# Optimization experiments

Hardware: AMD Instinct MI355X
Metric: run time of the kernel (lower is better)

The kernel has to match this reference:

```python
import jax, jax.numpy as jnp
import numpy as np

N = 100_000      # nodes
E = 1_600_000    # edges
IN, H, OUT = 128, 64, 32


def _gcn_edges(edge_index, n):
    """Add self-loops and compute symmetric GCN normalization (PyG gcn_norm)."""
    src, dst = edge_index[0], edge_index[1]
    loops = jnp.arange(n, dtype=src.dtype)
    src = jnp.concatenate([src, loops])
    dst = jnp.concatenate([dst, loops])
    deg = jax.ops.segment_sum(jnp.ones_like(dst, jnp.float32), dst, num_segments=n)
    dinv = jnp.where(deg > 0, jax.lax.rsqrt(deg), 0.0)
    norm = dinv[src] * dinv[dst]          # [E+N]
    return src, dst, norm


def _gcn_conv(x, src, dst, norm, W, b, n):
    h = x @ W.T                           # dense transform [n, out]
    msg = h[src] * norm[:, None]          # gather + scale per edge
    out = jax.ops.segment_sum(msg, dst, num_segments=n)  # scatter-add
    return out + b


def setup_inputs() -> dict:
    key = jax.random.key(0)
    k1, k2, k3, k4 = jax.random.split(key, 4)
    x = jax.random.normal(k1, (N, IN), dtype=jnp.float32)
    edge_index = jax.random.randint(k2, (2, E), 0, N, dtype=jnp.int32)
    # xavier_normal_: std = sqrt(2 / (fan_in + fan_out))
    W1 = jax.random.normal(k3, (H, IN), dtype=jnp.float32) * np.sqrt(2.0 / (IN + H))
    b1 = jnp.zeros((H,), dtype=jnp.float32)
    W2 = jax.random.normal(k4, (OUT, H), dtype=jnp.float32) * np.sqrt(2.0 / (H + OUT))
    b2 = jnp.zeros((OUT,), dtype=jnp.float32)
    return {"x": x, "edge_index": edge_index, "W1": W1, "b1": b1, "W2": W2, "b2": b2}


def reference(x, edge_index, W1, b1, W2, b2):
    n = x.shape[0]
    src, dst, norm = _gcn_edges(edge_index, n)
    h = _gcn_conv(x, src, dst, norm, W1, b1, n)
    h = jax.nn.relu(h)
    out = _gcn_conv(h, src, dst, norm, W2, b2, n)
    return out
```

## Files before the change

### kernel.cpp

```cpp
#include <hip/hip_runtime.h>

#define THREADS 256
#define G1 256
#define MAXNB 4096
#define BCAP 2688

using bf16x8 = __attribute__((ext_vector_type(8))) short;
using f32x4 = __attribute__((ext_vector_type(4))) float;

static __device__ __forceinline__ unsigned short f2bf(float f) {
  unsigned u = __float_as_uint(f);
  unsigned r = (u + 0x7fff + ((u >> 16) & 1)) >> 16;
  return (unsigned short)r;
}
static __device__ __forceinline__ float bflo(unsigned w) {
  return __uint_as_float(w << 16);
}
static __device__ __forceinline__ float bfhi(unsigned w) {
  return __uint_as_float(w & 0xffff0000u);
}
static __device__ __forceinline__ unsigned pk2(float a, float b) {
  return (unsigned)f2bf(a) | ((unsigned)f2bf(b) << 16);
}


__global__ void k_scan_chunk(const int* __restrict__ cnt, int* __restrict__ rp,
                             int* __restrict__ bsum, int m) {
  __shared__ int s[256];
  int b = blockIdx.x, t = threadIdx.x;
  int base = b * 1024 + t * 4;
  int v[4];
  int sum = 0;
#pragma unroll
  for (int k = 0; k < 4; ++k) {
    int i = base + k;
    v[k] = (i < m) ? cnt[i] : 0;
    sum += v[k];
  }
  s[t] = sum;
  __syncthreads();
  int mine = sum;
  for (int off = 1; off < 256; off <<= 1) {
    int y = (t >= off) ? s[t - off] : 0;
    __syncthreads();
    s[t] += y;
    __syncthreads();
  }
  int run = s[t] - mine;
  if (t == 255) bsum[b] = s[255];
#pragma unroll
  for (int k = 0; k < 4; ++k) {
    int i = base + k;
    if (i <= m) rp[i] = run;
    run += v[k];
  }
}

__global__ void k_scan_bsum(int* __restrict__ bsum, int nb) {
  __shared__ int s[256];
  int t = threadIdx.x;
  int v = (t < nb) ? bsum[t] : 0;
  s[t] = v;
  __syncthreads();
  for (int off = 1; off < 256; off <<= 1) {
    int y = (t >= off) ? s[t - off] : 0;
    __syncthreads();
    s[t] += y;
    __syncthreads();
  }
  if (t < nb) bsum[t] = s[t] - v;
}


__launch_bounds__(256)
__global__ void k_pcount(const int* __restrict__ dst, int* __restrict__ C, int e,
                         int NB, int chunk, unsigned* __restrict__ h1b,
                         unsigned* __restrict__ h2b, int n) {
  __shared__ int h[MAXNB];
  int blk = blockIdx.x, t = threadIdx.x;
  if (blk == 0) {
    if (t < 32) h1b[(size_t)n * 32 + t] = 0u;
    else if (t < 48) h2b[(size_t)n * 16 + (t - 32)] = 0u;
  }
  for (int i = t; i < NB; i += 256) h[i] = 0;
  __syncthreads();
  int beg = blk * chunk;
  int stop = min(e, beg + chunk);
  for (int j = beg + t; j < stop; j += 256) atomicAdd(&h[dst[j] >> 7], 1);
  __syncthreads();
  for (int i = t; i < NB; i += 256) C[i * G1 + blk] = h[i];
}

__launch_bounds__(256)
__global__ void k_partition(const int* __restrict__ src, const int* __restrict__ dst,
                            const int* __restrict__ Cs, const int* __restrict__ bsum,
                            int* __restrict__ bpack, int e, int NB, int chunk) {
  __shared__ int cur[MAXNB];
  int blk = blockIdx.x, t = threadIdx.x;
  for (int i = t; i < NB; i += 256) {
    int f = i * G1 + blk;
    cur[i] = Cs[f] + bsum[f >> 10];
  }
  __syncthreads();
  int beg = blk * chunk;
  int stop = min(e, beg + chunk);
  for (int j = beg + t; j < stop; j += 256) {
    int d = dst[j];
    int b = d >> 7;
    int pos = atomicAdd(&cur[b], 1);
    bpack[pos] = (src[j] << 7) | (d & 127);
  }
}

__launch_bounds__(256)
__global__ void k_bucket_csr(const int* __restrict__ bpack, const int* __restrict__ Cs,
                             const int* __restrict__ bsum, int* __restrict__ rp,
                             float* __restrict__ dinv, int* __restrict__ csr_src,
                             int n, int e, int NB) {
  __shared__ int cl[128];
  __shared__ int cur[128];
  __shared__ int buf[BCAP];
  int blk = blockIdx.x, t = threadIdx.x;
  int fb = blk * G1;
  int base = Cs[fb] + bsum[fb >> 10];
  int end;
  if (blk == NB - 1) {
    end = e;
  } else {
    int fe = (blk + 1) * G1;
    end = Cs[fe] + bsum[fe >> 10];
  }
  int cnt = end - base;
  if (t < 128) cl[t] = 0;
  __syncthreads();
  if (cnt <= BCAP) {
    for (int j = base + t; j < end; j += 256) {
      int p = bpack[j];
      buf[j - base] = p;
      atomicAdd(&cl[p & 127], 1);
    }
  } else {
    for (int j = base + t; j < end; j += 256) atomicAdd(&cl[bpack[j] & 127], 1);
  }
  __syncthreads();
  int own = (t < 128) ? cl[t] : 0;
  for (int off = 1; off < 128; off <<= 1) {
    int y = (t >= off && t < 128) ? cl[t - off] : 0;
    __syncthreads();
    if (t < 128) cl[t] += y;
    __syncthreads();
  }
  if (t < 128) {
    int excl = cl[t] - own;
    int v = (blk << 7) + t;
    if (v < n) {
      rp[v] = base + excl;
      dinv[v] = rsqrtf((float)own + 1.0f);
    }
    cur[t] = base + excl;
  }
  __syncthreads();
  if (cnt <= BCAP) {
    for (int j = t; j < cnt; j += 256) {
      int p = buf[j];
      int pos = atomicAdd(&cur[p & 127], 1);
      csr_src[pos] = p >> 7;
    }
  } else {
    for (int j = base + t; j < end; j += 256) {
      int p = bpack[j];
      int pos = atomicAdd(&cur[p & 127], 1);
      csr_src[pos] = p >> 7;
    }
  }
  if (blk == 0 && t == 0) rp[n] = e;
}


__launch_bounds__(256)
__global__ void k_gemm1(const float* __restrict__ x, const float* __restrict__ W1,
                        const float* __restrict__ dinv, unsigned short* __restrict__ h1b,
                        int n) {
  __shared__ uint4 sXb[64 * 16];
  __shared__ uint4 sWb[64 * 16];
  __shared__ __align__(16) unsigned short sOut[64 * 64];
  int t = threadIdx.x;
  const float4* x4 = (const float4*)x;
  const float4* W14 = (const float4*)W1;
  int rbase = blockIdx.x * 64;
#pragma unroll
  for (int p = 0; p < 4; ++p) {
    int q = t + 256 * p;
    int r = q >> 4, s = q & 15;
    int gr = rbase + r;
    float4 v0 = make_float4(0.f, 0.f, 0.f, 0.f), v1 = v0;
    if (gr < n) {
      v0 = x4[(size_t)gr * 32 + s * 2];
      v1 = x4[(size_t)gr * 32 + s * 2 + 1];
    }
    uint4 pk;
    pk.x = pk2(v0.x, v0.y);
    pk.y = pk2(v0.z, v0.w);
    pk.z = pk2(v1.x, v1.y);
    pk.w = pk2(v1.z, v1.w);
    sXb[r * 16 + (s ^ (r & 15))] = pk;
  }
#pragma unroll
  for (int p = 0; p < 4; ++p) {
    int q = t + 256 * p;
    int c = q >> 4, s = q & 15;
    float4 v0 = W14[c * 32 + s * 2];
    float4 v1 = W14[c * 32 + s * 2 + 1];
    uint4 pk;
    pk.x = pk2(v0.x, v0.y);
    pk.y = pk2(v0.z, v0.w);
    pk.z = pk2(v1.x, v1.y);
    pk.w = pk2(v1.z, v1.w);
    sWb[c * 16 + (s ^ (c & 15))] = pk;
  }
  __syncthreads();
  int lane = t & 63;
  int w = t >> 6;
  int l16 = lane & 15, quad = lane >> 4;
  int arow = w * 16 + l16;
  f32x4 acc0 = {0.f, 0.f, 0.f, 0.f};
  f32x4 acc1 = {0.f, 0.f, 0.f, 0.f};
  f32x4 acc2 = {0.f, 0.f, 0.f, 0.f};
  f32x4 acc3 = {0.f, 0.f, 0.f, 0.f};
#pragma unroll
  for (int kc = 0; kc < 4; ++kc) {
    int slot = kc * 4 + quad;
    uint4 ua = sXb[arow * 16 + (slot ^ (arow & 15))];
    bf16x8 a = *(bf16x8*)&ua;
    uint4 ub0 = sWb[(0 + l16) * 16 + (slot ^ l16)];
    uint4 ub1 = sWb[(16 + l16) * 16 + (slot ^ l16)];
    uint4 ub2 = sWb[(32 + l16) * 16 + (slot ^ l16)];
    uint4 ub3 = sWb[(48 + l16) * 16 + (slot ^ l16)];
    acc0 = __builtin_amdgcn_mfma_f32_16x16x32_bf16(a, *(bf16x8*)&ub0, acc0, 0, 0, 0);
    acc1 = __builtin_amdgcn_mfma_f32_16x16x32_bf16(a, *(bf16x8*)&ub1, acc1, 0, 0, 0);
    acc2 = __builtin_amdgcn_mfma_f32_16x16x32_bf16(a, *(bf16x8*)&ub2, acc2, 0, 0, 0);
    acc3 = __builtin_amdgcn_mfma_f32_16x16x32_bf16(a, *(bf16x8*)&ub3, acc3, 0, 0, 0);
  }
  float dvr[4];
#pragma unroll
  for (int r = 0; r < 4; ++r) {
    int grow = rbase + w * 16 + quad * 4 + r;
    dvr[r] = (grow < n) ? dinv[grow] : 0.f;
  }
#pragma unroll
  for (int r = 0; r < 4; ++r) {
    int rl = w * 16 + quad * 4 + r;
    sOut[rl * 64 + 0 + l16] = f2bf(acc0[r] * dvr[r]);
    sOut[rl * 64 + 16 + l16] = f2bf(acc1[r] * dvr[r]);
    sOut[rl * 64 + 32 + l16] = f2bf(acc2[r] * dvr[r]);
    sOut[rl * 64 + 48 + l16] = f2bf(acc3[r] * dvr[r]);
  }
  __syncthreads();
#pragma unroll
  for (int p = 0; p < 2; ++p) {
    int q = t + 256 * p;
    int r = q >> 3, s = q & 7;
    int gr = rbase + r;
    if (gr < n)
      *(uint4*)&h1b[(size_t)gr * 64 + s * 8] = *(uint4*)&sOut[r * 64 + s * 8];
  }
}


__launch_bounds__(256)
__global__ void k_agg1(const unsigned* __restrict__ h1p, const float* __restrict__ dinv,
                       const int* __restrict__ rp, const int* __restrict__ csr_src,
                       unsigned* __restrict__ agg1b, int n) {
  int gid = blockIdx.x * 256 + threadIdx.x;
  int v = gid >> 4, f4 = gid & 15;
  if (v >= n) return;
  const uint2* h1q = (const uint2*)h1p;
  int beg = rp[v], end = rp[v + 1];
  uint2 w0 = h1q[(size_t)v * 16 + f4];
  float acc[8][4];
#pragma unroll
  for (int k = 0; k < 8; ++k)
#pragma unroll
    for (int c = 0; c < 4; ++c) acc[k][c] = 0.f;
  acc[0][0] = bflo(w0.x);
  acc[0][1] = bfhi(w0.x);
  acc[0][2] = bflo(w0.y);
  acc[0][3] = bfhi(w0.y);
  for (int j = beg; j < end; j += 8) {
    int s[8];
#pragma unroll
    for (int k = 0; k < 8; ++k) s[k] = csr_src[j + k];
#pragma unroll
    for (int k = 1; k < 8; ++k) s[k] = (j + k < end) ? s[k] : n;
    uint2 g[8];
#pragma unroll
    for (int k = 0; k < 8; ++k) g[k] = h1q[(size_t)s[k] * 16 + f4];
#pragma unroll
    for (int k = 0; k < 8; ++k) {
      acc[k][0] += bflo(g[k].x);
      acc[k][1] += bfhi(g[k].x);
      acc[k][2] += bflo(g[k].y);
      acc[k][3] += bfhi(g[k].y);
    }
  }
  float s0 = ((acc[0][0] + acc[1][0]) + (acc[2][0] + acc[3][0])) +
             ((acc[4][0] + acc[5][0]) + (acc[6][0] + acc[7][0]));
  float s1 = ((acc[0][1] + acc[1][1]) + (acc[2][1] + acc[3][1])) +
             ((acc[4][1] + acc[5][1]) + (acc[6][1] + acc[7][1]));
  float s2 = ((acc[0][2] + acc[1][2]) + (acc[2][2] + acc[3][2])) +
             ((acc[4][2] + acc[5][2]) + (acc[6][2] + acc[7][2]));
  float s3 = ((acc[0][3] + acc[1][3]) + (acc[2][3] + acc[3][3])) +
             ((acc[4][3] + acc[5][3]) + (acc[6][3] + acc[7][3]));
  float dv = dinv[v];
  uint2 o;
  o.x = pk2(dv * s0, dv * s1);
  o.y = pk2(dv * s2, dv * s3);
  ((uint2*)agg1b)[(size_t)v * 16 + f4] = o;
}


__launch_bounds__(256)
__global__ void k_gemm2(const unsigned* __restrict__ agg1b, const float* __restrict__ b1,
                        const float* __restrict__ W2, const float* __restrict__ dinv,
                        unsigned short* __restrict__ h2b, int n) {
  __shared__ uint4 sXb[64 * 8];
  __shared__ uint4 sWb[32 * 8];
  __shared__ __align__(16) unsigned short sOut[64 * 32];
  int t = threadIdx.x;
  int rbase = blockIdx.x * 64;
  const uint4* a4 = (const uint4*)agg1b;
  const float4* b14 = (const float4*)b1;
  const float4* W24 = (const float4*)W2;
#pragma unroll
  for (int p = 0; p < 2; ++p) {
    int q = t + 256 * p;
    int r = q >> 3, s = q & 7;
    int gr = rbase + r;
    uint4 o = make_uint4(0u, 0u, 0u, 0u);
    if (gr < n) {
      uint4 a = a4[(size_t)gr * 8 + s];
      float4 blo = b14[s * 2], bhi = b14[s * 2 + 1];
      o.x = pk2(fmaxf(bflo(a.x) + blo.x, 0.f), fmaxf(bfhi(a.x) + blo.y, 0.f));
      o.y = pk2(fmaxf(bflo(a.y) + blo.z, 0.f), fmaxf(bfhi(a.y) + blo.w, 0.f));
      o.z = pk2(fmaxf(bflo(a.z) + bhi.x, 0.f), fmaxf(bfhi(a.z) + bhi.y, 0.f));
      o.w = pk2(fmaxf(bflo(a.w) + bhi.z, 0.f), fmaxf(bfhi(a.w) + bhi.w, 0.f));
    }
    sXb[r * 8 + (s ^ (r & 7))] = o;
  }
  {
    int c = t >> 3, s = t & 7;
    float4 v0 = W24[c * 16 + s * 2];
    float4 v1 = W24[c * 16 + s * 2 + 1];
    uint4 pk;
    pk.x = pk2(v0.x, v0.y);
    pk.y = pk2(v0.z, v0.w);
    pk.z = pk2(v1.x, v1.y);
    pk.w = pk2(v1.z, v1.w);
    sWb[c * 8 + (s ^ (c & 7))] = pk;
  }
  __syncthreads();
  int lane = t & 63;
  int w = t >> 6;
  int l16 = lane & 15, quad = lane >> 4;
  int arow = w * 16 + l16;
  f32x4 acc0 = {0.f, 0.f, 0.f, 0.f};
  f32x4 acc1 = {0.f, 0.f, 0.f, 0.f};
#pragma unroll
  for (int kc = 0; kc < 2; ++kc) {
    int slot = kc * 4 + quad;
    uint4 ua = sXb[arow * 8 + (slot ^ (arow & 7))];
    bf16x8 a = *(bf16x8*)&ua;
    uint4 ub0 = sWb[l16 * 8 + (slot ^ (l16 & 7))];
    uint4 ub1 = sWb[(16 + l16) * 8 + (slot ^ (l16 & 7))];
    acc0 = __builtin_amdgcn_mfma_f32_16x16x32_bf16(a, *(bf16x8*)&ub0, acc0, 0, 0, 0);
    acc1 = __builtin_amdgcn_mfma_f32_16x16x32_bf16(a, *(bf16x8*)&ub1, acc1, 0, 0, 0);
  }
  float dvr[4];
#pragma unroll
  for (int r = 0; r < 4; ++r) {
    int grow = rbase + w * 16 + quad * 4 + r;
    dvr[r] = (grow < n) ? dinv[grow] : 0.f;
  }
#pragma unroll
  for (int r = 0; r < 4; ++r) {
    int rl = w * 16 + quad * 4 + r;
    sOut[rl * 32 + l16] = f2bf(acc0[r] * dvr[r]);
    sOut[rl * 32 + 16 + l16] = f2bf(acc1[r] * dvr[r]);
  }
  __syncthreads();
  {
    int r = t >> 2, s = t & 3;
    int gr = rbase + r;
    if (gr < n)
      *(uint4*)&h2b[(size_t)gr * 32 + s * 8] = *(uint4*)&sOut[r * 32 + s * 8];
  }
}


__launch_bounds__(256)
__global__ void k_agg2(const unsigned* __restrict__ h2p, const float* __restrict__ dinv,
                       const int* __restrict__ rp, const int* __restrict__ csr_src,
                       const float* __restrict__ b2, float* __restrict__ out, int n) {
  int gid = blockIdx.x * 256 + threadIdx.x;
  int v = gid >> 3, f4 = gid & 7;
  if (v >= n) return;
  const uint2* h2q = (const uint2*)h2p;
  int beg = rp[v], end = rp[v + 1];
  uint2 w0 = h2q[(size_t)v * 8 + f4];
  float acc[8][4];
#pragma unroll
  for (int k = 0; k < 8; ++k)
#pragma unroll
    for (int c = 0; c < 4; ++c) acc[k][c] = 0.f;
  acc[0][0] = bflo(w0.x);
  acc[0][1] = bfhi(w0.x);
  acc[0][2] = bflo(w0.y);
  acc[0][3] = bfhi(w0.y);
  for (int j = beg; j < end; j += 8) {
    int s[8];
#pragma unroll
    for (int k = 0; k < 8; ++k) s[k] = csr_src[j + k];
#pragma unroll
    for (int k = 1; k < 8; ++k) s[k] = (j + k < end) ? s[k] : n;
    uint2 g[8];
#pragma unroll
    for (int k = 0; k < 8; ++k) g[k] = h2q[(size_t)s[k] * 8 + f4];
#pragma unroll
    for (int k = 0; k < 8; ++k) {
      acc[k][0] += bflo(g[k].x);
      acc[k][1] += bfhi(g[k].x);
      acc[k][2] += bflo(g[k].y);
      acc[k][3] += bfhi(g[k].y);
    }
  }
  float s0 = ((acc[0][0] + acc[1][0]) + (acc[2][0] + acc[3][0])) +
             ((acc[4][0] + acc[5][0]) + (acc[6][0] + acc[7][0]));
  float s1 = ((acc[0][1] + acc[1][1]) + (acc[2][1] + acc[3][1])) +
             ((acc[4][1] + acc[5][1]) + (acc[6][1] + acc[7][1]));
  float s2 = ((acc[0][2] + acc[1][2]) + (acc[2][2] + acc[3][2])) +
             ((acc[4][2] + acc[5][2]) + (acc[6][2] + acc[7][2]));
  float s3 = ((acc[0][3] + acc[1][3]) + (acc[2][3] + acc[3][3])) +
             ((acc[4][3] + acc[5][3]) + (acc[6][3] + acc[7][3]));
  float dv = dinv[v];
  float4 bv = ((const float4*)b2)[f4];
  float4 o;
  o.x = fmaf(dv, s0, bv.x);
  o.y = fmaf(dv, s1, bv.y);
  o.z = fmaf(dv, s2, bv.z);
  o.w = fmaf(dv, s3, bv.w);
  ((float4*)out)[(size_t)v * 8 + f4] = o;
}


extern "C" void kernel_launch(void* const* d_in, const int* in_sizes, int n_in,
                              void* d_out, int out_size, void* d_ws, size_t ws_size,
                              hipStream_t stream) {
  const float* x = (const float*)d_in[0];
  const int* ei = (const int*)d_in[1];
  const float* W1 = (const float*)d_in[2];
  const float* b1 = (const float*)d_in[3];
  const float* W2 = (const float*)d_in[4];
  const float* b2 = (const float*)d_in[5];
  float* out = (float*)d_out;

  const int n = in_sizes[0] / 128;
  const int e = in_sizes[1] / 2;
  const int* src = ei;
  const int* dst = ei + e;

  const int NB = (n + 127) >> 7;
  const int m = NB * G1;
  const int chunk = (e + G1 - 1) / G1;
  const int NC = (m + 1 + 1023) / 1024;

  char* base = (char*)d_ws;
  size_t off = 0;
  auto alloc = [&](size_t bytes) {
    char* p = base + off;
    off = (off + bytes + 255) & ~(size_t)255;
    return p;
  };
  int* C = (int*)alloc((size_t)m * 4);
  int* Cs = (int*)alloc((size_t)(m + 1) * 4);
  int* bsum = (int*)alloc(1024 * 4);
  int* bpack = (int*)alloc((size_t)e * 4);
  int* rp = (int*)alloc((size_t)(n + 1) * 4);
  int* csr_src = (int*)alloc((size_t)(e + 8) * 4);
  float* dinv = (float*)alloc((size_t)n * 4);
  unsigned short* h1b = (unsigned short*)alloc((size_t)(n + 1) * 64 * 2);
  unsigned* agg1b = (unsigned*)alloc((size_t)n * 64 * 2);
  unsigned short* h2b = (unsigned short*)alloc((size_t)(n + 1) * 32 * 2);

  k_pcount<<<G1, 256, 0, stream>>>(dst, C, e, NB, chunk, (unsigned*)h1b,
                                   (unsigned*)h2b, n);
  k_scan_chunk<<<NC, 256, 0, stream>>>(C, Cs, bsum, m);
  k_scan_bsum<<<1, 256, 0, stream>>>(bsum, NC);
  k_partition<<<G1, 256, 0, stream>>>(src, dst, Cs, bsum, bpack, e, NB, chunk);
  k_bucket_csr<<<NB, 256, 0, stream>>>(bpack, Cs, bsum, rp, dinv, csr_src, n, e, NB);

  k_gemm1<<<(n + 63) / 64, 256, 0, stream>>>(x, W1, dinv, h1b, n);
  {
    long long total = (long long)n * 16;
    k_agg1<<<(int)((total + 255) / 256), 256, 0, stream>>>((const unsigned*)h1b, dinv,
                                                           rp, csr_src, agg1b, n);
  }

  k_gemm2<<<(n + 63) / 64, 256, 0, stream>>>(agg1b, b1, W2, dinv, h2b, n);
  {
    long long total = (long long)n * 8;
    k_agg2<<<(int)((total + 255) / 256), 256, 0, stream>>>((const unsigned*)h2b, dinv,
                                                           rp, csr_src, b2, out, n);
  }
}
```

Baseline: 209.7 us.

## Fuse all GCN stages into one persistent kernel with software grid barriers

```diff
diff --git a/kernel.cpp b/kernel.cpp
--- a/kernel.cpp
+++ b/kernel.cpp
@@ -1,7 +1,6 @@
 #include <hip/hip_runtime.h>
 
-#define THREADS 256
-#define G1 256
+#define GP 256
 #define MAXNB 4096
 #define BCAP 2688
 
@@ -23,432 +22,459 @@
   return (unsigned)f2bf(a) | ((unsigned)f2bf(b) << 16);
 }
 
-
-__global__ void k_scan_chunk(const int* __restrict__ cnt, int* __restrict__ rp,
-                             int* __restrict__ bsum, int m) {
-  __shared__ int s[256];
-  int b = blockIdx.x, t = threadIdx.x;
-  int base = b * 1024 + t * 4;
-  int v[4];
-  int sum = 0;
-#pragma unroll
-  for (int k = 0; k < 4; ++k) {
-    int i = base + k;
-    v[k] = (i < m) ? cnt[i] : 0;
-    sum += v[k];
-  }
-  s[t] = sum;
+static __device__ __forceinline__ void gridbar(int* cnt, int target) {
   __syncthreads();
-  int mine = sum;
-  for (int off = 1; off < 256; off <<= 1) {
-    int y = (t >= off) ? s[t - off] : 0;
+  if (threadIdx.x == 0) {
+    __threadfence();
+    __hip_atomic_fetch_add(cnt, 1, __ATOMIC_RELAXED, __HIP_MEMORY_SCOPE_AGENT);
+    while (__hip_atomic_load(cnt, __ATOMIC_RELAXED, __HIP_MEMORY_SCOPE_AGENT) <
+           target)
+      __builtin_amdgcn_s_sleep(2);
+    __threadfence();
+  }
+  __syncthreads();
+}
+
+
+__global__ void __launch_bounds__(256) k_mega(
+    const float* __restrict__ x, const int* __restrict__ src,
+    const int* __restrict__ dst, const float* __restrict__ W1,
+    const float* __restrict__ b1, const float* __restrict__ W2,
+    const float* __restrict__ b2, int* __restrict__ C, int* __restrict__ Cs,
+    int* __restrict__ bsum, int* __restrict__ bpack, int* __restrict__ rp,
+    int* __restrict__ csr_src, float* __restrict__ dinv,
+    unsigned short* __restrict__ h1b, unsigned short* __restrict__ h2b,
+    float* __restrict__ out, int* __restrict__ barcnt, int n, int e, int NB, int m,
+    int NC, int chunk) {
+  __shared__ __align__(16) char lds_raw[32 * 1024];
+  const int t = threadIdx.x;
+  const int blk = blockIdx.x;
+  const int G = gridDim.x;
+  int bphase = 0;
+
+  if (blk == 0) {
+    unsigned* h1u = (unsigned*)h1b;
+    unsigned* h2u = (unsigned*)h2b;
+    if (t < 32) h1u[(size_t)n * 32 + t] = 0u;
+    else if (t < 48) h2u[(size_t)n * 16 + (t - 32)] = 0u;
+  }
+  {
+    int* h = (int*)lds_raw;
+    for (int pb = blk; pb < GP; pb += G) {
+      __syncthreads();
+      for (int i = t; i < NB; i += 256) h[i] = 0;
+      __syncthreads();
+      int beg = pb * chunk;
+      int stop = min(e, beg + chunk);
+      for (int j = beg + t; j < stop; j += 256) atomicAdd(&h[dst[j] >> 7], 1);
+      __syncthreads();
+      for (int i = t; i < NB; i += 256) C[i * GP + pb] = h[i];
+    }
+  }
+  gridbar(barcnt, ++bphase * G);
+
+  {
+    int* s = (int*)lds_raw;
+    for (int c = blk; c < NC; c += G) {
+      __syncthreads();
+      int base = c * 1024 + t * 4;
+      int v[4];
+      int sum = 0;
+#pragma unroll
+      for (int k = 0; k < 4; ++k) {
+        int i = base + k;
+        v[k] = (i < m) ? C[i] : 0;
+        sum += v[k];
+      }
+      s[t] = sum;
+      __syncthreads();
+      int mine = sum;
+      for (int off = 1; off < 256; off <<= 1) {
+        int y = (t >= off) ? s[t - off] : 0;
+        __syncthreads();
+        s[t] += y;
+        __syncthreads();
+      }
+      int run = s[t] - mine;
+      if (t == 255) bsum[c] = s[255];
+#pragma unroll
+      for (int k = 0; k < 4; ++k) {
+        int i = base + k;
+        if (i <= m) Cs[i] = run;
+        run += v[k];
+      }
+    }
+  }
+  gridbar(barcnt, ++bphase * G);
+
+  int* sb = (int*)lds_raw;
+  {
+    int* ss = sb + 1024;
+    int v4[4];
+    int b4 = t * 4;
+    int sum = 0;
+#pragma unroll
+    for (int k = 0; k < 4; ++k) {
+      int i = b4 + k;
+      v4[k] = (i < NC) ? bsum[i] : 0;
+      sum += v4[k];
+    }
+    ss[t] = sum;
     __syncthreads();
-    s[t] += y;
+    int mine = sum;
+    for (int off = 1; off < 256; off <<= 1) {
+      int y = (t >= off) ? ss[t - off] : 0;
+      __syncthreads();
+      ss[t] += y;
+      __syncthreads();
+    }
+    int run = ss[t] - mine;
+#pragma unroll
+    for (int k = 0; k < 4; ++k) {
+      int i = b4 + k;
+      if (i < NC) sb[i] = run;
+      run += v4[k];
+    }
     __syncthreads();
   }
-  int run = s[t] - mine;
-  if (t == 255) bsum[b] = s[255];
-#pragma unroll
-  for (int k = 0; k < 4; ++k) {
-    int i = base + k;
-    if (i <= m) rp[i] = run;
-    run += v[k];
-  }
-}
-
-__global__ void k_scan_bsum(int* __restrict__ bsum, int nb) {
-  __shared__ int s[256];
-  int t = threadIdx.x;
-  int v = (t < nb) ? bsum[t] : 0;
-  s[t] = v;
-  __syncthreads();
-  for (int off = 1; off < 256; off <<= 1) {
-    int y = (t >= off) ? s[t - off] : 0;
-    __syncthreads();
-    s[t] += y;
-    __syncthreads();
-  }
-  if (t < nb) bsum[t] = s[t] - v;
-}
-
-
-__launch_bounds__(256)
-__global__ void k_pcount(const int* __restrict__ dst, int* __restrict__ C, int e,
-                         int NB, int chunk, unsigned* __restrict__ h1b,
-                         unsigned* __restrict__ h2b, int n) {
-  __shared__ int h[MAXNB];
-  int blk = blockIdx.x, t = threadIdx.x;
-  if (blk == 0) {
-    if (t < 32) h1b[(size_t)n * 32 + t] = 0u;
-    else if (t < 48) h2b[(size_t)n * 16 + (t - 32)] = 0u;
-  }
-  for (int i = t; i < NB; i += 256) h[i] = 0;
-  __syncthreads();
-  int beg = blk * chunk;
-  int stop = min(e, beg + chunk);
-  for (int j = beg + t; j < stop; j += 256) atomicAdd(&h[dst[j] >> 7], 1);
-  __syncthreads();
-  for (int i = t; i < NB; i += 256) C[i * G1 + blk] = h[i];
-}
-
-__launch_bounds__(256)
-__global__ void k_partition(const int* __restrict__ src, const int* __restrict__ dst,
-                            const int* __restrict__ Cs, const int* __restrict__ bsum,
-                            int* __restrict__ bpack, int e, int NB, int chunk) {
-  __shared__ int cur[MAXNB];
-  int blk = blockIdx.x, t = threadIdx.x;
-  for (int i = t; i < NB; i += 256) {
-    int f = i * G1 + blk;
-    cur[i] = Cs[f] + bsum[f >> 10];
-  }
-  __syncthreads();
-  int beg = blk * chunk;
-  int stop = min(e, beg + chunk);
-  for (int j = beg + t; j < stop; j += 256) {
-    int d = dst[j];
-    int b = d >> 7;
-    int pos = atomicAdd(&cur[b], 1);
-    bpack[pos] = (src[j] << 7) | (d & 127);
-  }
-}
-
-__launch_bounds__(256)
-__global__ void k_bucket_csr(const int* __restrict__ bpack, const int* __restrict__ Cs,
-                             const int* __restrict__ bsum, int* __restrict__ rp,
-                             float* __restrict__ dinv, int* __restrict__ csr_src,
-                             int n, int e, int NB) {
-  __shared__ int cl[128];
-  __shared__ int cur[128];
-  __shared__ int buf[BCAP];
-  int blk = blockIdx.x, t = threadIdx.x;
-  int fb = blk * G1;
-  int base = Cs[fb] + bsum[fb >> 10];
-  int end;
-  if (blk == NB - 1) {
-    end = e;
-  } else {
-    int fe = (blk + 1) * G1;
-    end = Cs[fe] + bsum[fe >> 10];
-  }
-  int cnt = end - base;
-  if (t < 128) cl[t] = 0;
-  __syncthreads();
-  if (cnt <= BCAP) {
-    for (int j = base + t; j < end; j += 256) {
-      int p = bpack[j];
-      buf[j - base] = p;
-      atomicAdd(&cl[p & 127], 1);
-    }
-  } else {
-    for (int j = base + t; j < end; j += 256) atomicAdd(&cl[bpack[j] & 127], 1);
-  }
-  __syncthreads();
-  int own = (t < 128) ? cl[t] : 0;
-  for (int off = 1; off < 128; off <<= 1) {
-    int y = (t >= off && t < 128) ? cl[t - off] : 0;
-    __syncthreads();
-    if (t < 128) cl[t] += y;
-    __syncthreads();
-  }
-  if (t < 128) {
-    int excl = cl[t] - own;
-    int v = (blk << 7) + t;
-    if (v < n) {
-      rp[v] = base + excl;
-      dinv[v] = rsqrtf((float)own + 1.0f);
-    }
-    cur[t] = base + excl;
-  }
-  __syncthreads();
-  if (cnt <= BCAP) {
-    for (int j = t; j < cnt; j += 256) {
-      int p = buf[j];
-      int pos = atomicAdd(&cur[p & 127], 1);
-      csr_src[pos] = p >> 7;
-    }
-  } else {
-    for (int j = base + t; j < end; j += 256) {
-      int p = bpack[j];
-      int pos = atomicAdd(&cur[p & 127], 1);
-      csr_src[pos] = p >> 7;
-    }
-  }
-  if (blk == 0 && t == 0) rp[n] = e;
-}
-
-
-__launch_bounds__(256)
-__global__ void k_gemm1(const float* __restrict__ x, const float* __restrict__ W1,
-                        const float* __restrict__ dinv, unsigned short* __restrict__ h1b,
-                        int n) {
-  __shared__ uint4 sXb[64 * 16];
-  __shared__ uint4 sWb[64 * 16];
-  __shared__ __align__(16) unsigned short sOut[64 * 64];
-  int t = threadIdx.x;
-  const float4* x4 = (const float4*)x;
-  const float4* W14 = (const float4*)W1;
-  int rbase = blockIdx.x * 64;
-#pragma unroll
-  for (int p = 0; p < 4; ++p) {
-    int q = t + 256 * p;
-    int r = q >> 4, s = q & 15;
-    int gr = rbase + r;
-    float4 v0 = make_float4(0.f, 0.f, 0.f, 0.f), v1 = v0;
-    if (gr < n) {
-      v0 = x4[(size_t)gr * 32 + s * 2];
-      v1 = x4[(size_t)gr * 32 + s * 2 + 1];
-    }
-    uint4 pk;
-    pk.x = pk2(v0.x, v0.y);
-    pk.y = pk2(v0.z, v0.w);
-    pk.z = pk2(v1.x, v1.y);
-    pk.w = pk2(v1.z, v1.w);
-    sXb[r * 16 + (s ^ (r & 15))] = pk;
-  }
-#pragma unroll
-  for (int p = 0; p < 4; ++p) {
-    int q = t + 256 * p;
-    int c = q >> 4, s = q & 15;
-    float4 v0 = W14[c * 32 + s * 2];
-    float4 v1 = W14[c * 32 + s * 2 + 1];
-    uint4 pk;
-    pk.x = pk2(v0.x, v0.y);
-    pk.y = pk2(v0.z, v0.w);
-    pk.z = pk2(v1.x, v1.y);
-    pk.w = pk2(v1.z, v1.w);
-    sWb[c * 16 + (s ^ (c & 15))] = pk;
-  }
-  __syncthreads();
-  int lane = t & 63;
-  int w = t >> 6;
-  int l16 = lane & 15, quad = lane >> 4;
-  int arow = w * 16 + l16;
-  f32x4 acc0 = {0.f, 0.f, 0.f, 0.f};
-  f32x4 acc1 = {0.f, 0.f, 0.f, 0.f};
-  f32x4 acc2 = {0.f, 0.f, 0.f, 0.f};
-  f32x4 acc3 = {0.f, 0.f, 0.f, 0.f};
-#pragma unroll
-  for (int kc = 0; kc < 4; ++kc) {
-    int slot = kc * 4 + quad;
-    uint4 ua = sXb[arow * 16 + (slot ^ (arow & 15))];
-    bf16x8 a = *(bf16x8*)&ua;
-    uint4 ub0 = sWb[(0 + l16) * 16 + (slot ^ l16)];
-    uint4 ub1 = sWb[(16 + l16) * 16 + (slot ^ l16)];
-    uint4 ub2 = sWb[(32 + l16) * 16 + (slot ^ l16)];
-    uint4 ub3 = sWb[(48 + l16) * 16 + (slot ^ l16)];
-    acc0 = __builtin_amdgcn_mfma_f32_16x16x32_bf16(a, *(bf16x8*)&ub0, acc0, 0, 0, 0);
-    acc1 = __builtin_amdgcn_mfma_f32_16x16x32_bf16(a, *(bf16x8*)&ub1, acc1, 0, 0, 0);
-    acc2 = __builtin_amdgcn_mfma_f32_16x16x32_bf16(a, *(bf16x8*)&ub2, acc2, 0, 0, 0);
-    acc3 = __builtin_amdgcn_mfma_f32_16x16x32_bf16(a, *(bf16x8*)&ub3, acc3, 0, 0, 0);
-  }
-  float dvr[4];
-#pragma unroll
-  for (int r = 0; r < 4; ++r) {
-    int grow = rbase + w * 16 + quad * 4 + r;
-    dvr[r] = (grow < n) ? dinv[grow] : 0.f;
-  }
-#pragma unroll
-  for (int r = 0; r < 4; ++r) {
-    int rl = w * 16 + quad * 4 + r;
-    sOut[rl * 64 + 0 + l16] = f2bf(acc0[r] * dvr[r]);
-    sOut[rl * 64 + 16 + l16] = f2bf(acc1[r] * dvr[r]);
-    sOut[rl * 64 + 32 + l16] = f2bf(acc2[r] * dvr[r]);
-    sOut[rl * 64 + 48 + l16] = f2bf(acc3[r] * dvr[r]);
-  }
-  __syncthreads();
-#pragma unroll
-  for (int p = 0; p < 2; ++p) {
-    int q = t + 256 * p;
-    int r = q >> 3, s = q & 7;
-    int gr = rbase + r;
-    if (gr < n)
-      *(uint4*)&h1b[(size_t)gr * 64 + s * 8] = *(uint4*)&sOut[r * 64 + s * 8];
-  }
-}
-
-
-__launch_bounds__(256)
-__global__ void k_agg1(const unsigned* __restrict__ h1p, const float* __restrict__ dinv,
-                       const int* __restrict__ rp, const int* __restrict__ csr_src,
-                       unsigned* __restrict__ agg1b, int n) {
-  int gid = blockIdx.x * 256 + threadIdx.x;
-  int v = gid >> 4, f4 = gid & 15;
-  if (v >= n) return;
-  const uint2* h1q = (const uint2*)h1p;
-  int beg = rp[v], end = rp[v + 1];
-  uint2 w0 = h1q[(size_t)v * 16 + f4];
-  float acc[8][4];
-#pragma unroll
-  for (int k = 0; k < 8; ++k)
-#pragma unroll
-    for (int c = 0; c < 4; ++c) acc[k][c] = 0.f;
-  acc[0][0] = bflo(w0.x);
-  acc[0][1] = bfhi(w0.x);
-  acc[0][2] = bflo(w0.y);
-  acc[0][3] = bfhi(w0.y);
-  for (int j = beg; j < end; j += 8) {
-    int s[8];
-#pragma unroll
-    for (int k = 0; k < 8; ++k) s[k] = csr_src[j + k];
-#pragma unroll
-    for (int k = 1; k < 8; ++k) s[k] = (j + k < end) ? s[k] : n;
-    uint2 g[8];
-#pragma unroll
-    for (int k = 0; k < 8; ++k) g[k] = h1q[(size_t)s[k] * 16 + f4];
-#pragma unroll
-    for (int k = 0; k < 8; ++k) {
-      acc[k][0] += bflo(g[k].x);
-      acc[k][1] += bfhi(g[k].x);
-      acc[k][2] += bflo(g[k].y);
-      acc[k][3] += bfhi(g[k].y);
-    }
-  }
-  float s0 = ((acc[0][0] + acc[1][0]) + (acc[2][0] + acc[3][0])) +
-             ((acc[4][0] + acc[5][0]) + (acc[6][0] + acc[7][0]));
-  float s1 = ((acc[0][1] + acc[1][1]) + (acc[2][1] + acc[3][1])) +
-             ((acc[4][1] + acc[5][1]) + (acc[6][1] + acc[7][1]));
-  float s2 = ((acc[0][2] + acc[1][2]) + (acc[2][2] + acc[3][2])) +
-             ((acc[4][2] + acc[5][2]) + (acc[6][2] + acc[7][2]));
-  float s3 = ((acc[0][3] + acc[1][3]) + (acc[2][3] + acc[3][3])) +
-             ((acc[4][3] + acc[5][3]) + (acc[6][3] + acc[7][3]));
-  float dv = dinv[v];
-  uint2 o;
-  o.x = pk2(dv * s0, dv * s1);
-  o.y = pk2(dv * s2, dv * s3);
-  ((uint2*)agg1b)[(size_t)v * 16 + f4] = o;
-}
-
-
-__launch_bounds__(256)
-__global__ void k_gemm2(const unsigned* __restrict__ agg1b, const float* __restrict__ b1,
-                        const float* __restrict__ W2, const float* __restrict__ dinv,
-                        unsigned short* __restrict__ h2b, int n) {
-  __shared__ uint4 sXb[64 * 8];
-  __shared__ uint4 sWb[32 * 8];
-  __shared__ __align__(16) unsigned short sOut[64 * 32];
-  int t = threadIdx.x;
-  int rbase = blockIdx.x * 64;
-  const uint4* a4 = (const uint4*)agg1b;
-  const float4* b14 = (const float4*)b1;
-  const float4* W24 = (const float4*)W2;
-#pragma unroll
-  for (int p = 0; p < 2; ++p) {
-    int q = t + 256 * p;
-    int r = q >> 3, s = q & 7;
-    int gr = rbase + r;
-    uint4 o = make_uint4(0u, 0u, 0u, 0u);
-    if (gr < n) {
-      uint4 a = a4[(size_t)gr * 8 + s];
-      float4 blo = b14[s * 2], bhi = b14[s * 2 + 1];
-      o.x = pk2(fmaxf(bflo(a.x) + blo.x, 0.f), fmaxf(bfhi(a.x) + blo.y, 0.f));
-      o.y = pk2(fmaxf(bflo(a.y) + blo.z, 0.f), fmaxf(bfhi(a.y) + blo.w, 0.f));
-      o.z = pk2(fmaxf(bflo(a.z) + bhi.x, 0.f), fmaxf(bfhi(a.z) + bhi.y, 0.f));
-      o.w = pk2(fmaxf(bflo(a.w) + bhi.z, 0.f), fmaxf(bfhi(a.w) + bhi.w, 0.f));
-    }
-    sXb[r * 8 + (s ^ (r & 7))] = o;
-  }
-  {
-    int c = t >> 3, s = t & 7;
-    float4 v0 = W24[c * 16 + s * 2];
-    float4 v1 = W24[c * 16 + s * 2 + 1];
-    uint4 pk;
-    pk.x = pk2(v0.x, v0.y);
-    pk.y = pk2(v0.z, v0.w);
-    pk.z = pk2(v1.x, v1.y);
-    pk.w = pk2(v1.z, v1.w);
-    sWb[c * 8 + (s ^ (c & 7))] = pk;
-  }
-  __syncthreads();
-  int lane = t & 63;
-  int w = t >> 6;
-  int l16 = lane & 15, quad = lane >> 4;
-  int arow = w * 16 + l16;
-  f32x4 acc0 = {0.f, 0.f, 0.f, 0.f};
-  f32x4 acc1 = {0.f, 0.f, 0.f, 0.f};
-#pragma unroll
-  for (int kc = 0; kc < 2; ++kc) {
-    int slot = kc * 4 + quad;
-    uint4 ua = sXb[arow * 8 + (slot ^ (arow & 7))];
-    bf16x8 a = *(bf16x8*)&ua;
-    uint4 ub0 = sWb[l16 * 8 + (slot ^ (l16 & 7))];
-    uint4 ub1 = sWb[(16 + l16) * 8 + (slot ^ (l16 & 7))];
-    acc0 = __builtin_amdgcn_mfma_f32_16x16x32_bf16(a, *(bf16x8*)&ub0, acc0, 0, 0, 0);
-    acc1 = __builtin_amdgcn_mfma_f32_16x16x32_bf16(a, *(bf16x8*)&ub1, acc1, 0, 0, 0);
-  }
-  float dvr[4];
-#pragma unroll
-  for (int r = 0; r < 4; ++r) {
-    int grow = rbase + w * 16 + quad * 4 + r;
-    dvr[r] = (grow < n) ? dinv[grow] : 0.f;
-  }
-#pragma unroll
-  for (int r = 0; r < 4; ++r) {
-    int rl = w * 16 + quad * 4 + r;
-    sOut[rl * 32 + l16] = f2bf(acc0[r] * dvr[r]);
-    sOut[rl * 32 + 16 + l16] = f2bf(acc1[r] * dvr[r]);
-  }
-  __syncthreads();
-  {
-    int r = t >> 2, s = t & 3;
-    int gr = rbase + r;
-    if (gr < n)
-      *(uint4*)&h2b[(size_t)gr * 32 + s * 8] = *(uint4*)&sOut[r * 32 + s * 8];
-  }
-}
-
-
-__launch_bounds__(256)
-__global__ void k_agg2(const unsigned* __restrict__ h2p, const float* __restrict__ dinv,
-                       const int* __restrict__ rp, const int* __restrict__ csr_src,
-                       const float* __restrict__ b2, float* __restrict__ out, int n) {
-  int gid = blockIdx.x * 256 + threadIdx.x;
-  int v = gid >> 3, f4 = gid & 7;
-  if (v >= n) return;
-  const uint2* h2q = (const uint2*)h2p;
-  int beg = rp[v], end = rp[v + 1];
-  uint2 w0 = h2q[(size_t)v * 8 + f4];
-  float acc[8][4];
-#pragma unroll
-  for (int k = 0; k < 8; ++k)
-#pragma unroll
-    for (int c = 0; c < 4; ++c) acc[k][c] = 0.f;
-  acc[0][0] = bflo(w0.x);
-  acc[0][1] = bfhi(w0.x);
-  acc[0][2] = bflo(w0.y);
-  acc[0][3] = bfhi(w0.y);
-  for (int j = beg; j < end; j += 8) {
-    int s[8];
-#pragma unroll
-    for (int k = 0; k < 8; ++k) s[k] = csr_src[j + k];
-#pragma unroll
-    for (int k = 1; k < 8; ++k) s[k] = (j + k < end) ? s[k] : n;
-    uint2 g[8];
-#pragma unroll
-    for (int k = 0; k < 8; ++k) g[k] = h2q[(size_t)s[k] * 8 + f4];
-#pragma unroll
-    for (int k = 0; k < 8; ++k) {
-      acc[k][0] += bflo(g[k].x);
-      acc[k][1] += bfhi(g[k].x);
-      acc[k][2] += bflo(g[k].y);
-      acc[k][3] += bfhi(g[k].y);
-    }
-  }
-  float s0 = ((acc[0][0] + acc[1][0]) + (acc[2][0] + acc[3][0])) +
-             ((acc[4][0] + acc[5][0]) + (acc[6][0] + acc[7][0]));
-  float s1 = ((acc[0][1] + acc[1][1]) + (acc[2][1] + acc[3][1])) +
-             ((acc[4][1] + acc[5][1]) + (acc[6][1] + acc[7][1]));
-  float s2 = ((acc[0][2] + acc[1][2]) + (acc[2][2] + acc[3][2])) +
-             ((acc[4][2] + acc[5][2]) + (acc[6][2] + acc[7][2]));
-  float s3 = ((acc[0][3] + acc[1][3]) + (acc[2][3] + acc[3][3])) +
-             ((acc[4][3] + acc[5][3]) + (acc[6][3] + acc[7][3]));
-  float dv = dinv[v];
-  float4 bv = ((const float4*)b2)[f4];
-  float4 o;
-  o.x = fmaf(dv, s0, bv.x);
-  o.y = fmaf(dv, s1, bv.y);
-  o.z = fmaf(dv, s2, bv.z);
-  o.w = fmaf(dv, s3, bv.w);
-  ((float4*)out)[(size_t)v * 8 + f4] = o;
+
+  {
+    int* cur = (int*)lds_raw + 1280;
+    for (int pb = blk; pb < GP; pb += G) {
+      __syncthreads();
+      for (int i = t; i < NB; i += 256) {
+        int f = i * GP + pb;
+        cur[i] = Cs[f] + sb[f >> 10];
+      }
+      __syncthreads();
+      int beg = pb * chunk;
+      int stop = min(e, beg + chunk);
+      for (int j = beg + t; j < stop; j += 256) {
+        int d = dst[j];
+        int b = d >> 7;
+        int pos = atomicAdd(&cur[b], 1);
+        bpack[pos] = (src[j] << 7) | (d & 127);
+      }
+    }
+  }
+  gridbar(barcnt, ++bphase * G);
+
+  {
+    int* cl = (int*)lds_raw + 1280;
+    int* cur = cl + 128;
+    int* buf = cur + 128;
+    if (blk == 0 && t == 0) rp[n] = e;
+    for (int b = blk; b < NB; b += G) {
+      __syncthreads();
+      int fb = b * GP;
+      int base = Cs[fb] + sb[fb >> 10];
+      int end2 = (b == NB - 1) ? e : (Cs[fb + GP] + sb[(fb + GP) >> 10]);
+      int cnt = end2 - base;
+      if (t < 128) cl[t] = 0;
+      __syncthreads();
+      if (cnt <= BCAP) {
+        for (int j = base + t; j < end2; j += 256) {
+          int p = bpack[j];
+          buf[j - base] = p;
+          atomicAdd(&cl[p & 127], 1);
+        }
+      } else {
+        for (int j = base + t; j < end2; j += 256) atomicAdd(&cl[bpack[j] & 127], 1);
+      }
+      __syncthreads();
+      int own = (t < 128) ? cl[t] : 0;
+      for (int off = 1; off < 128; off <<= 1) {
+        int y = (t >= off && t < 128) ? cl[t - off] : 0;
+        __syncthreads();
+        if (t < 128) cl[t] += y;
+        __syncthreads();
+      }
+      if (t < 128) {
+        int excl = cl[t] - own;
+        int v = (b << 7) + t;
+        if (v < n) {
+          rp[v] = base + excl;
+          dinv[v] = rsqrtf((float)own + 1.0f);
+        }
+        cur[t] = base + excl;
+      }
+      __syncthreads();
+      if (cnt <= BCAP) {
+        for (int j = t; j < cnt; j += 256) {
+          int p = buf[j];
+          int pos = atomicAdd(&cur[p & 127], 1);
+          csr_src[pos] = p >> 7;
+        }
+      } else {
+        for (int j = base + t; j < end2; j += 256) {
+          int p = bpack[j];
+          int pos = atomicAdd(&cur[p & 127], 1);
+          csr_src[pos] = p >> 7;
+        }
+      }
+    }
+  }
+  gridbar(barcnt, ++bphase * G);
+
+  {
+    uint4* sXb = (uint4*)lds_raw;
+    uint4* sWb = sXb + 1024;
+    unsigned short* sOut = (unsigned short*)lds_raw;
+    const float4* x4 = (const float4*)x;
+    const float4* W14 = (const float4*)W1;
+#pragma unroll
+    for (int p = 0; p < 4; ++p) {
+      int q = t + 256 * p;
+      int c = q >> 4, s2 = q & 15;
+      float4 v0 = W14[c * 32 + s2 * 2];
+      float4 v1 = W14[c * 32 + s2 * 2 + 1];
+      uint4 pk;
+      pk.x = pk2(v0.x, v0.y);
+      pk.y = pk2(v0.z, v0.w);
+      pk.z = pk2(v1.x, v1.y);
+      pk.w = pk2(v1.z, v1.w);
+      sWb[c * 16 + (s2 ^ (c & 15))] = pk;
+    }
+    for (int tile = blk; tile * 64 < n; tile += G) {
+      int rbase = tile * 64;
+      __syncthreads();
+#pragma unroll
+      for (int p = 0; p < 4; ++p) {
+        int q = t + 256 * p;
+        int r = q >> 4, s2 = q & 15;
+        int gr = rbase + r;
+        float4 v0 = make_float4(0.f, 0.f, 0.f, 0.f), v1 = v0;
+        if (gr < n) {
+          v0 = x4[(size_t)gr * 32 + s2 * 2];
+          v1 = x4[(size_t)gr * 32 + s2 * 2 + 1];
+        }
+        uint4 pk;
+        pk.x = pk2(v0.x, v0.y);
+        pk.y = pk2(v0.z, v0.w);
+        pk.z = pk2(v1.x, v1.y);
+        pk.w = pk2(v1.z, v1.w);
+        sXb[r * 16 + (s2 ^ (r & 15))] = pk;
+      }
+      __syncthreads();
+      int lane = t & 63;
+      int w = t >> 6;
+      int l16 = lane & 15, quad = lane >> 4;
+      int arow = w * 16 + l16;
+      f32x4 acc0 = {0.f, 0.f, 0.f, 0.f};
+      f32x4 acc1 = {0.f, 0.f, 0.f, 0.f};
+      f32x4 acc2 = {0.f, 0.f, 0.f, 0.f};
+      f32x4 acc3 = {0.f, 0.f, 0.f, 0.f};
+#pragma unroll
+      for (int kc = 0; kc < 4; ++kc) {
+        int slot = kc * 4 + quad;
+        uint4 ua = sXb[arow * 16 + (slot ^ (arow & 15))];
+        bf16x8 a = *(bf16x8*)&ua;
+        uint4 ub0 = sWb[(0 + l16) * 16 + (slot ^ l16)];
+        uint4 ub1 = sWb[(16 + l16) * 16 + (slot ^ l16)];
+        uint4 ub2 = sWb[(32 + l16) * 16 + (slot ^ l16)];
+        uint4 ub3 = sWb[(48 + l16) * 16 + (slot ^ l16)];
+        acc0 = __builtin_amdgcn_mfma_f32_16x16x32_bf16(a, *(bf16x8*)&ub0, acc0, 0, 0, 0);
+        acc1 = __builtin_amdgcn_mfma_f32_16x16x32_bf16(a, *(bf16x8*)&ub1, acc1, 0, 0, 0);
+        acc2 = __builtin_amdgcn_mfma_f32_16x16x32_bf16(a, *(bf16x8*)&ub2, acc2, 0, 0, 0);
+        acc3 = __builtin_amdgcn_mfma_f32_16x16x32_bf16(a, *(bf16x8*)&ub3, acc3, 0, 0, 0);
+      }
+      float dvr[4];
+#pragma unroll
+      for (int r = 0; r < 4; ++r) {
+        int grow = rbase + w * 16 + quad * 4 + r;
+        dvr[r] = (grow < n) ? dinv[grow] : 0.f;
+      }
+      __syncthreads();
+#pragma unroll
+      for (int r = 0; r < 4; ++r) {
+        int rl = w * 16 + quad * 4 + r;
+        sOut[rl * 64 + 0 + l16] = f2bf(acc0[r] * dvr[r]);
+        sOut[rl * 64 + 16 + l16] = f2bf(acc1[r] * dvr[r]);
+        sOut[rl * 64 + 32 + l16] = f2bf(acc2[r] * dvr[r]);
+        sOut[rl * 64 + 48 + l16] = f2bf(acc3[r] * dvr[r]);
+      }
+      __syncthreads();
+#pragma unroll
+      for (int p = 0; p < 2; ++p) {
+        int q = t + 256 * p;
+        int r = q >> 3, s2 = q & 7;
+        int gr = rbase + r;
+        if (gr < n)
+          *(uint4*)&h1b[(size_t)gr * 64 + s2 * 8] = *(uint4*)&sOut[r * 64 + s2 * 8];
+      }
+    }
+  }
+  gridbar(barcnt, ++bphase * G);
+
+  {
+    uint4* sXb2 = (uint4*)lds_raw;
+    uint4* sWb2 = sXb2 + 512;
+    unsigned short* sOut2 = (unsigned short*)(sWb2 + 256);
+    const uint2* h1q = (const uint2*)h1b;
+    const float4* W24 = (const float4*)W2;
+    const float4* b14 = (const float4*)b1;
+    {
+      int c = t >> 3, s2 = t & 7;
+      float4 v0 = W24[c * 16 + s2 * 2];
+      float4 v1 = W24[c * 16 + s2 * 2 + 1];
+      uint4 pk;
+      pk.x = pk2(v0.x, v0.y);
+      pk.y = pk2(v0.z, v0.w);
+      pk.z = pk2(v1.x, v1.y);
+      pk.w = pk2(v1.z, v1.w);
+      sWb2[c * 8 + (s2 ^ (c & 7))] = pk;
+    }
+    int f4 = t & 15;
+    int rloc = t >> 4;
+    for (int tile = blk; tile * 64 < n; tile += G) {
+      int rbase = tile * 64;
+      __syncthreads();
+#pragma unroll
+      for (int sub = 0; sub < 4; ++sub) {
+        int r = sub * 16 + rloc;
+        int v = rbase + r;
+        float r0 = 0.f, r1 = 0.f, r2 = 0.f, r3 = 0.f;
+        if (v < n) {
+          int beg = rp[v], end = rp[v + 1];
+          uint2 w0 = h1q[(size_t)v * 16 + f4];
+          float acc[8][4];
+#pragma unroll
+          for (int k = 0; k < 8; ++k)
+#pragma unroll
+            for (int c = 0; c < 4; ++c) acc[k][c] = 0.f;
+          acc[0][0] = bflo(w0.x);
+          acc[0][1] = bfhi(w0.x);
+          acc[0][2] = bflo(w0.y);
+          acc[0][3] = bfhi(w0.y);
+          for (int j = beg; j < end; j += 8) {
+            int s[8];
+#pragma unroll
+            for (int k = 0; k < 8; ++k) s[k] = csr_src[j + k];
+#pragma unroll
+            for (int k = 1; k < 8; ++k) s[k] = (j + k < end) ? s[k] : n;
+            uint2 g[8];
+#pragma unroll
+            for (int k = 0; k < 8; ++k) g[k] = h1q[(size_t)s[k] * 16 + f4];
+#pragma unroll
+            for (int k = 0; k < 8; ++k) {
+              acc[k][0] += bflo(g[k].x);
+              acc[k][1] += bfhi(g[k].x);
+              acc[k][2] += bflo(g[k].y);
+              acc[k][3] += bfhi(g[k].y);
+            }
+          }
+          float s0 = ((acc[0][0] + acc[1][0]) + (acc[2][0] + acc[3][0])) +
+                     ((acc[4][0] + acc[5][0]) + (acc[6][0] + acc[7][0]));
+          float s1 = ((acc[0][1] + acc[1][1]) + (acc[2][1] + acc[3][1])) +
+                     ((acc[4][1] + acc[5][1]) + (acc[6][1] + acc[7][1]));
+          float s2 = ((acc[0][2] + acc[1][2]) + (acc[2][2] + acc[3][2])) +
+                     ((acc[4][2] + acc[5][2]) + (acc[6][2] + acc[7][2]));
+          float s3 = ((acc[0][3] + acc[1][3]) + (acc[2][3] + acc[3][3])) +
+                     ((acc[4][3] + acc[5][3]) + (acc[6][3] + acc[7][3]));
+          float dv = dinv[v];
+          float4 bb = b14[f4];
+          r0 = fmaxf(fmaf(dv, s0, bb.x), 0.f);
+          r1 = fmaxf(fmaf(dv, s1, bb.y), 0.f);
+          r2 = fmaxf(fmaf(dv, s2, bb.z), 0.f);
+          r3 = fmaxf(fmaf(dv, s3, bb.w), 0.f);
+        }
+        unsigned u0 = pk2(r0, r1), u1 = pk2(r2, r3);
+        unsigned* xb = (unsigned*)sXb2;
+        int slot = (f4 >> 1) ^ (r & 7);
+        xb[(r * 8 + slot) * 4 + (f4 & 1) * 2 + 0] = u0;
+        xb[(r * 8 + slot) * 4 + (f4 & 1) * 2 + 1] = u1;
+      }
+      __syncthreads();
+      int lane = t & 63;
+      int w = t >> 6;
+      int l16 = lane & 15, quad = lane >> 4;
+      int arow = w * 16 + l16;
+      f32x4 acc0 = {0.f, 0.f, 0.f, 0.f};
+      f32x4 acc1 = {0.f, 0.f, 0.f, 0.f};
+#pragma unroll
+      for (int kc = 0; kc < 2; ++kc) {
+        int slot = kc * 4 + quad;
+        uint4 ua = sXb2[arow * 8 + (slot ^ (arow & 7))];
+        bf16x8 a = *(bf16x8*)&ua;
+        uint4 ub0 = sWb2[l16 * 8 + (slot ^ (l16 & 7))];
+        uint4 ub1 = sWb2[(16 + l16) * 8 + (slot ^ (l16 & 7))];
+        acc0 = __builtin_amdgcn_mfma_f32_16x16x32_bf16(a, *(bf16x8*)&ub0, acc0, 0, 0, 0);
+        acc1 = __builtin_amdgcn_mfma_f32_16x16x32_bf16(a, *(bf16x8*)&ub1, acc1, 0, 0, 0);
+      }
+      float dvr[4];
+#pragma unroll
+      for (int r = 0; r < 4; ++r) {
+        int grow = rbase + w * 16 + quad * 4 + r;
+        dvr[r] = (grow < n) ? dinv[grow] : 0.f;
+      }
+#pragma unroll
+      for (int r = 0; r < 4; ++r) {
+        int rl = w * 16 + quad * 4 + r;
+        sOut2[rl * 32 + l16] = f2bf(acc0[r] * dvr[r]);
+        sOut2[rl * 32 + 16 + l16] = f2bf(acc1[r] * dvr[r]);
+      }
+      __syncthreads();
+      {
+        int r = t >> 2, s2 = t & 3;
+        int gr = rbase + r;
+        if (gr < n)
+          *(uint4*)&h2b[(size_t)gr * 32 + s2 * 8] = *(uint4*)&sOut2[r * 32 + s2 * 8];
+      }
+    }
+  }
+  gridbar(barcnt, ++bphase * G);
+
+  {
+    const uint2* h2q = (const uint2*)h2b;
+    int total = n * 8;
+    for (int g8 = blk * 256 + t; g8 < total; g8 += G * 256) {
+      int v = g8 >> 3, f4 = g8 & 7;
+      int beg = rp[v], end = rp[v + 1];
+      uint2 w0 = h2q[(size_t)v * 8 + f4];
+      float acc[8][4];
+#pragma unroll
+      for (int k = 0; k < 8; ++k)
+#pragma unroll
+        for (int c = 0; c < 4; ++c) acc[k][c] = 0.f;
+      acc[0][0] = bflo(w0.x);
+      acc[0][1] = bfhi(w0.x);
+      acc[0][2] = bflo(w0.y);
+      acc[0][3] = bfhi(w0.y);
+      for (int j = beg; j < end; j += 8) {
+        int s[8];
+#pragma unroll
+        for (int k = 0; k < 8; ++k) s[k] = csr_src[j + k];
+#pragma unroll
+        for (int k = 1; k < 8; ++k) s[k] = (j + k < end) ? s[k] : n;
+        uint2 g[8];
+#pragma unroll
+        for (int k = 0; k < 8; ++k) g[k] = h2q[(size_t)s[k] * 8 + f4];
+#pragma unroll
+        for (int k = 0; k < 8; ++k) {
+          acc[k][0] += bflo(g[k].x);
+          acc[k][1] += bfhi(g[k].x);
+          acc[k][2] += bflo(g[k].y);
+          acc[k][3] += bfhi(g[k].y);
+        }
+      }
+      float s0 = ((acc[0][0] + acc[1][0]) + (acc[2][0] + acc[3][0])) +
+                 ((acc[4][0] + acc[5][0]) + (acc[6][0] + acc[7][0]));
+      float s1 = ((acc[0][1] + acc[1][1]) + (acc[2][1] + acc[3][1])) +
+                 ((acc[4][1] + acc[5][1]) + (acc[6][1] + acc[7][1]));
+      float s2 = ((acc[0][2] + acc[1][2]) + (acc[2][2] + acc[3][2])) +
+                 ((acc[4][2] + acc[5][2]) + (acc[6][2] + acc[7][2]));
+      float s3 = ((acc[0][3] + acc[1][3]) + (acc[2][3] + acc[3][3])) +
+                 ((acc[4][3] + acc[5][3]) + (acc[6][3] + acc[7][3]));
+      float dv = dinv[v];
+      float4 bv = ((const float4*)b2)[f4];
+      float4 o;
+      o.x = fmaf(dv, s0, bv.x);
+      o.y = fmaf(dv, s1, bv.y);
+      o.z = fmaf(dv, s2, bv.z);
+      o.w = fmaf(dv, s3, bv.w);
+      ((float4*)out)[(size_t)v * 8 + f4] = o;
+    }
+  }
 }
 
 
@@ -469,8 +495,8 @@
   const int* dst = ei + e;
 
   const int NB = (n + 127) >> 7;
-  const int m = NB * G1;
-  const int chunk = (e + G1 - 1) / G1;
+  const int m = NB * GP;
+  const int chunk = (e + GP - 1) / GP;
   const int NC = (m + 1 + 1023) / 1024;
 
   char* base = (char*)d_ws;
@@ -488,27 +514,27 @@
   int* csr_src = (int*)alloc((size_t)(e + 8) * 4);
   float* dinv = (float*)alloc((size_t)n * 4);
   unsigned short* h1b = (unsigned short*)alloc((size_t)(n + 1) * 64 * 2);
-  unsigned* agg1b = (unsigned*)alloc((size_t)n * 64 * 2);
   unsigned short* h2b = (unsigned short*)alloc((size_t)(n + 1) * 32 * 2);
-
-  k_pcount<<<G1, 256, 0, stream>>>(dst, C, e, NB, chunk, (unsigned*)h1b,
-                                   (unsigned*)h2b, n);
-  k_scan_chunk<<<NC, 256, 0, stream>>>(C, Cs, bsum, m);
-  k_scan_bsum<<<1, 256, 0, stream>>>(bsum, NC);
-  k_partition<<<G1, 256, 0, stream>>>(src, dst, Cs, bsum, bpack, e, NB, chunk);
-  k_bucket_csr<<<NB, 256, 0, stream>>>(bpack, Cs, bsum, rp, dinv, csr_src, n, e, NB);
-
-  k_gemm1<<<(n + 63) / 64, 256, 0, stream>>>(x, W1, dinv, h1b, n);
-  {
-    long long total = (long long)n * 16;
-    k_agg1<<<(int)((total + 255) / 256), 256, 0, stream>>>((const unsigned*)h1b, dinv,
-                                                           rp, csr_src, agg1b, n);
-  }
-
-  k_gemm2<<<(n + 63) / 64, 256, 0, stream>>>(agg1b, b1, W2, dinv, h2b, n);
-  {
-    long long total = (long long)n * 8;
-    k_agg2<<<(int)((total + 255) / 256), 256, 0, stream>>>((const unsigned*)h2b, dinv,
-                                                           rp, csr_src, b2, out, n);
-  }
-}
+  int* barcnt = (int*)alloc(256);
+
+  static int s_grid = 0;
+  if (s_grid == 0) {
+    int bpc = 0;
+    hipError_t err = hipOccupancyMaxActiveBlocksPerMultiprocessor(&bpc, k_mega, 256, 0);
+    int cu = 256;
+    hipDeviceProp_t prop;
+    if (hipGetDeviceProperties(&prop, 0) == hipSuccess &&
+        prop.multiProcessorCount > 0)
+      cu = prop.multiProcessorCount;
+    if (err != hipSuccess || bpc < 1) bpc = 1;
+    long long g = (long long)bpc * cu;
+    if (g > 1024) g = 1024;
+    if (g < 1) g = 1;
+    s_grid = (int)g;
+  }
+
+  hipMemsetAsync(barcnt, 0, 256, stream);
+  k_mega<<<s_grid, 256, 0, stream>>>(x, src, dst, W1, b1, W2, b2, C, Cs, bsum, bpack,
+                                     rp, csr_src, dinv, h1b, h2b, out, barcnt, n, e,
+                                     NB, m, NC, chunk);
+}
```

Measured after the change: 569.4 us. 172% more time.
